# Kernel tuning notes

Measured on AMD Instinct MI355X. Metric: run time of the kernel, lower is better.

The kernel has to match this reference:

```python
import jax, jax.numpy as jnp
import numpy as np

IN_DIM = 256
HIDDEN = 512
MEM = 256
IN_LEN = 4096
THETA = 4096.0
BATCH = 32


def _expm(M):
    # scaling-and-squaring with Taylor series (float64)
    nrm = max(np.linalg.norm(M, 1), 1e-30)
    s = max(0, int(np.ceil(np.log2(nrm))) + 1)
    A = M / (2.0 ** s)
    d = M.shape[0]
    E = np.eye(d)
    term = np.eye(d)
    for k in range(1, 30):
        term = term @ A / k
        E = E + term
    for _ in range(s):
        E = E @ E
    return E


def _gen_AB(memory_size, theta):
    Q = np.arange(memory_size, dtype=np.float64).reshape(-1, 1)
    R = (2 * Q + 1) / theta
    i, j = np.meshgrid(Q, Q, indexing='ij')
    A = np.where(i < j, -1.0, (-1.0) ** (i - j + 1)) * R
    B = (-1.0) ** Q * R  # [mem, 1]
    # ZOH discretization with dt=1: expm of augmented [[A,B],[0,0]]
    d = memory_size
    em = np.zeros((d + 1, d + 1))
    em[:d, :d] = A
    em[:d, d:] = B
    ed = _expm(em)
    Ad = ed[:d, :d]
    Bd = ed[:d, d:]
    return Ad, Bd


def _impulse(memory_size, in_len, theta):
    Ad, Bd = _gen_AB(memory_size, theta)
    H = np.empty((memory_size, in_len), dtype=np.float64)
    v = Bd.copy()  # [mem, 1]
    for t in range(in_len):
        H[:, t] = v[:, 0]
        v = Ad @ v
    return H.astype(np.float32)


def setup_inputs() -> dict:
    key = jax.random.key(0)
    kx, ku, kh = jax.random.split(key, 3)
    x = jax.random.normal(kx, (BATCH, IN_LEN, IN_DIM), dtype=jnp.float32)
    W_u = jax.random.normal(ku, (1, IN_DIM), dtype=jnp.float32)
    W_h = jax.random.normal(kh, (HIDDEN, MEM + IN_DIM), dtype=jnp.float32)
    H = jnp.asarray(_impulse(MEM, IN_LEN, THETA))  # [mem, in_len]
    return {"x": x, "W_u": W_u, "W_h": W_h, "H": H}


def reference(x, W_u, W_h, H):
    batch, n, _ = x.shape
    # encode: u = relu(x @ W_u^T)  -> [B, n, 1]
    u = jax.nn.relu(jnp.einsum('bni,oi->bno', x, W_u))
    # FFT long convolution with impulse response H
    u_fft = jnp.fft.rfft(u.transpose(0, 2, 1), n=2 * n, axis=-1)  # [B,1,n+1]
    H_fft = jnp.fft.rfft(H, n=2 * n, axis=-1)                      # [mem,n+1]
    m = jnp.fft.irfft(u_fft * H_fft[None], n=2 * n, axis=-1)       # [B,mem,2n]
    m = m[:, :, :n].transpose(0, 2, 1)                             # [B,n,mem]
    # output head: h = relu([m, x] @ W_h^T)
    input_h = jnp.concatenate((m, x), axis=-1)                     # [B,n,mem+in_dim]
    h = jax.nn.relu(jnp.einsum('bnc,oc->bno', input_h, W_h))       # [B,n,hidden]
    h_n = h[:, -1, :]
    return (h, h_n)
```

## Files before the change

### kernel.cpp

```cpp
#include <hip/hip_runtime.h>
#include <hip/hip_bf16.h>
#include <math.h>


#define BATCH 32
#define T     4096
#define IND   256
#define HID   512
#define MEM   256
#define FFT_N 8192
#define FFT_LOG 13
#define BT    131072

typedef __attribute__((ext_vector_type(8))) short short8;
typedef __attribute__((ext_vector_type(8))) _Float16 half8;
typedef __attribute__((ext_vector_type(4))) float f32x4;

__device__ inline short f2bf(float f) {
    unsigned u = __float_as_uint(f);
    unsigned r = (u + 0x7FFFu + ((u >> 16) & 1u)) >> 16;
    return (short)r;
}
__device__ inline short f2h(float f) {
    union { _Float16 h; short s; } u;
    u.h = (_Float16)f;
    return u.s;
}

__global__ __launch_bounds__(256) void relu_u_kernel(const float* __restrict__ x,
                                                     const float* __restrict__ Wu,
                                                     float* __restrict__ u) {
    int wave = threadIdx.x >> 6, lane = threadIdx.x & 63;
    int r = blockIdx.x * 4 + wave;
    const float4 xv = *(const float4*)(x + (size_t)r * IND + lane * 4);
    const float4 wv = *(const float4*)(Wu + lane * 4);
    float acc = xv.x * wv.x + xv.y * wv.y + xv.z * wv.z + xv.w * wv.w;
    for (int off = 32; off; off >>= 1) acc += __shfl_down(acc, off);
    if (lane == 0) u[r] = fmaxf(acc, 0.f);
}

__device__ void fft_fwd_r4(float* re, float* im) {
    __syncthreads();
    {
        const float fm = -(float)M_PI / 4096.f;
#pragma unroll
        for (int s = 0; s < 8; ++s) {
            int k = threadIdx.x + s * 512;
            float sn, cs; __sincosf(fm * (float)k, &sn, &cs);
            float ar = re[k], ai = im[k], br = re[k + 4096], bi = im[k + 4096];
            re[k] = ar + br; im[k] = ai + bi;
            float dr = ar - br, di = ai - bi;
            re[k + 4096] = cs * dr - sn * di;
            im[k + 4096] = cs * di + sn * dr;
        }
        __syncthreads();
    }
#pragma unroll
    for (int st = 10; st >= 0; st -= 2) {
        int q = 1 << st;
        float fm = -(float)M_PI / (float)(2 * q);
#pragma unroll
        for (int s = 0; s < 4; ++s) {
            int k = threadIdx.x + s * 512;
            int j = k & (q - 1);
            int i0 = ((k >> st) << (st + 2)) + j;
            float ar = re[i0],         ai = im[i0];
            float br = re[i0 + q],     bi = im[i0 + q];
            float cr = re[i0 + 2 * q], ci = im[i0 + 2 * q];
            float dr = re[i0 + 3 * q], di = im[i0 + 3 * q];
            float t0r = ar + cr, t0i = ai + ci;
            float t1r = ar - cr, t1i = ai - ci;
            float t2r = br + dr, t2i = bi + di;
            float t3r = bi - di, t3i = dr - br;
            float sn, cs; __sincosf(fm * (float)j, &sn, &cs);
            float w2r = cs * cs - sn * sn, w2i = 2.f * cs * sn;
            float w3r = w2r * cs - w2i * sn, w3i = w2r * sn + w2i * cs;
            re[i0] = t0r + t2r;               im[i0] = t0i + t2i;
            float er = t0r - t2r, ei = t0i - t2i;
            re[i0 + q] = er * w2r - ei * w2i; im[i0 + q] = er * w2i + ei * w2r;
            float fr = t1r + t3r, fi = t1i + t3i;
            re[i0 + 2 * q] = fr * cs - fi * sn; im[i0 + 2 * q] = fr * sn + fi * cs;
            float gr = t1r - t3r, gi = t1i - t3i;
            re[i0 + 3 * q] = gr * w3r - gi * w3i; im[i0 + 3 * q] = gr * w3i + gi * w3r;
        }
        __syncthreads();
    }
}
__device__ void fft_inv_r4(float* re, float* im) {
    __syncthreads();
#pragma unroll
    for (int st = 0; st <= 10; st += 2) {
        int q = 1 << st;
        float fm = (float)M_PI / (float)(2 * q);
#pragma unroll
        for (int s = 0; s < 4; ++s) {
            int k = threadIdx.x + s * 512;
            int j = k & (q - 1);
            int i0 = ((k >> st) << (st + 2)) + j;
            float Ar = re[i0],         Ai = im[i0];
            float Br = re[i0 + q],     Bi = im[i0 + q];
            float Cr = re[i0 + 2 * q], Ci = im[i0 + 2 * q];
            float Dr = re[i0 + 3 * q], Di = im[i0 + 3 * q];
            float sn, cs; __sincosf(fm * (float)j, &sn, &cs);
            float w2r = cs * cs - sn * sn, w2i = 2.f * cs * sn;
            float w3r = w2r * cs - w2i * sn, w3i = w2r * sn + w2i * cs;
            float bpr = Br * w2r - Bi * w2i, bpi = Br * w2i + Bi * w2r;
            float cpr = Cr * cs - Ci * sn,   cpi = Cr * sn + Ci * cs;
            float dpr = Dr * w3r - Di * w3i, dpi = Dr * w3i + Di * w3r;
            float t0r = Ar + bpr, t0i = Ai + bpi;
            float t2r = Ar - bpr, t2i = Ai - bpi;
            float t1r = cpr + dpr, t1i = cpi + dpi;
            float t3r = cpr - dpr, t3i = cpi - dpi;
            re[i0]         = t0r + t1r; im[i0]         = t0i + t1i;
            re[i0 + 2 * q] = t0r - t1r; im[i0 + 2 * q] = t0i - t1i;
            re[i0 + q]     = t2r - t3i; im[i0 + q]     = t2i + t3r;
            re[i0 + 3 * q] = t2r + t3i; im[i0 + 3 * q] = t2i - t3r;
        }
        __syncthreads();
    }
    {
        const float fm = (float)M_PI / 4096.f;
#pragma unroll
        for (int s = 0; s < 8; ++s) {
            int k = threadIdx.x + s * 512;
            float sn, cs; __sincosf(fm * (float)k, &sn, &cs);
            float br = re[k + 4096], bi = im[k + 4096];
            float tr = cs * br - sn * bi, ti = cs * bi + sn * br;
            float ar = re[k], ai = im[k];
            re[k] = ar + tr;        im[k] = ai + ti;
            re[k + 4096] = ar - tr; im[k + 4096] = ai - ti;
        }
        __syncthreads();
    }
}

__global__ __launch_bounds__(512) void fwd_all_kernel(const float* __restrict__ u,
                                                      const float* __restrict__ H,
                                                      float2* __restrict__ Uf,
                                                      float2* __restrict__ Hf) {
    __shared__ float re[FFT_N];
    __shared__ float im[FFT_N];
    int r = blockIdx.x;
    const float* src = (r < BATCH) ? (u + (size_t)r * T) : (H + (size_t)(r - BATCH) * T);
    float2* dst = (r < BATCH) ? (Uf + (size_t)r * FFT_N) : (Hf + (size_t)(r - BATCH) * FFT_N);
    for (int i = threadIdx.x; i < FFT_N; i += 512) {
        re[i] = (i < T) ? src[i] : 0.f;
        im[i] = 0.f;
    }
    fft_fwd_r4(re, im);
    for (int i = threadIdx.x; i < FFT_N; i += 512) dst[i] = make_float2(re[i], im[i]);
}

__global__ __launch_bounds__(512) void conv_m_kernel(const float2* __restrict__ Uf,
                                                     const float2* __restrict__ Hf,
                                                     float* __restrict__ mT) {
    int p = blockIdx.x;
    int b = blockIdx.y;
    __shared__ float re[FFT_N];
    __shared__ float im[FFT_N];
    const float2* Ub = Uf + (size_t)b * FFT_N;
    const float2* H0 = Hf + (size_t)(2 * p) * FFT_N;
    const float2* H1 = Hf + (size_t)(2 * p + 1) * FFT_N;
    for (int f = threadIdx.x; f < FFT_N; f += 512) {
        float2 uv = Ub[f], h0 = H0[f], h1 = H1[f];
        float gr = h0.x - h1.y, gi = h0.y + h1.x;
        re[f] = uv.x * gr - uv.y * gi;
        im[f] = uv.x * gi + uv.y * gr;
    }
    fft_inv_r4(re, im);
    const float inv = 1.0f / (float)FFT_N;
    float* m0 = mT + (size_t)(2 * p) * BT + (size_t)b * T;
    float* m1 = mT + (size_t)(2 * p + 1) * BT + (size_t)b * T;
    for (int t = threadIdx.x; t < T; t += 512) {
        m0[t] = re[t] * inv;
        m1[t] = im[t] * inv;
    }
}

__global__ __launch_bounds__(256) void h_gemm_kernel(const float* __restrict__ x,
                                                     const float* __restrict__ Wh,
                                                     const float* __restrict__ mT,
                                                     float* __restrict__ out) {
    __shared__ __align__(16) short Asl[4][128][8];
    __shared__ __align__(16) short Bsl[4][128][8];
    int bn = blockIdx.x;
    int bm = blockIdx.y;
    int t = threadIdx.x;
    int wv = t >> 6, lane = t & 63;
    int wm = (wv & 1) * 64, wn = (wv >> 1) * 64;
    int ln = lane & 15, kg = lane >> 4;

    f32x4 acc[4][4] = {};
    int mrow = t >> 1, khalf = t & 1;
    for (int kc = 0; kc < HID; kc += 32) {
        float va[16];
        if (kc < MEM) {
            const float* mb = mT + (size_t)(kc + khalf * 16) * BT + (size_t)bm * 128 + mrow;
#pragma unroll
            for (int d = 0; d < 16; ++d) va[d] = mb[(size_t)d * BT];
        } else {
            const float* xr = x + (size_t)(bm * 128 + mrow) * IND + (kc - MEM) + khalf * 16;
            float4 v0 = *(const float4*)(xr + 0);
            float4 v1 = *(const float4*)(xr + 4);
            float4 v2 = *(const float4*)(xr + 8);
            float4 v3 = *(const float4*)(xr + 12);
            va[0] = v0.x; va[1] = v0.y; va[2] = v0.z; va[3] = v0.w;
            va[4] = v1.x; va[5] = v1.y; va[6] = v1.z; va[7] = v1.w;
            va[8] = v2.x; va[9] = v2.y; va[10] = v2.z; va[11] = v2.w;
            va[12] = v3.x; va[13] = v3.y; va[14] = v3.z; va[15] = v3.w;
        }
        short8 s0 = { f2h(va[0]), f2h(va[1]), f2h(va[2]), f2h(va[3]),
                      f2h(va[4]), f2h(va[5]), f2h(va[6]), f2h(va[7]) };
        short8 s1 = { f2h(va[8]), f2h(va[9]), f2h(va[10]), f2h(va[11]),
                      f2h(va[12]), f2h(va[13]), f2h(va[14]), f2h(va[15]) };
        const float* wr = Wh + (size_t)(bn * 128 + mrow) * HID + kc + khalf * 16;
        float4 w0 = *(const float4*)(wr + 0);
        float4 w1 = *(const float4*)(wr + 4);
        float4 w2 = *(const float4*)(wr + 8);
        float4 w3 = *(const float4*)(wr + 12);
        short8 b0 = { f2h(w0.x), f2h(w0.y), f2h(w0.z), f2h(w0.w),
                      f2h(w1.x), f2h(w1.y), f2h(w1.z), f2h(w1.w) };
        short8 b1 = { f2h(w2.x), f2h(w2.y), f2h(w2.z), f2h(w2.w),
                      f2h(w3.x), f2h(w3.y), f2h(w3.z), f2h(w3.w) };
        __syncthreads();
        *(short8*)&Asl[khalf * 2 + 0][mrow][0] = s0;
        *(short8*)&Asl[khalf * 2 + 1][mrow][0] = s1;
        *(short8*)&Bsl[khalf * 2 + 0][mrow][0] = b0;
        *(short8*)&Bsl[khalf * 2 + 1][mrow][0] = b1;
        __syncthreads();
        half8 af[4], bfr[4];
#pragma unroll
        for (int i = 0; i < 4; ++i) af[i] = *(half8*)&Asl[kg][wm + i * 16 + ln][0];
#pragma unroll
        for (int j = 0; j < 4; ++j) bfr[j] = *(half8*)&Bsl[kg][wn + j * 16 + ln][0];
#pragma unroll
        for (int i = 0; i < 4; ++i)
#pragma unroll
            for (int j = 0; j < 4; ++j)
                acc[i][j] = __builtin_amdgcn_mfma_f32_16x16x32_f16(af[i], bfr[j], acc[i][j], 0, 0, 0);
    }
#pragma unroll
    for (int i = 0; i < 4; ++i) {
#pragma unroll
        for (int j = 0; j < 4; ++j) {
#pragma unroll
            for (int r = 0; r < 4; ++r) {
                int row = bm * 128 + wm + i * 16 + (lane >> 4) * 4 + r;
                int col = bn * 128 + wn + j * 16 + ln;
                float v = fmaxf(acc[i][j][r], 0.f);
                out[(size_t)row * HID + col] = v;
                if ((row & (T - 1)) == (T - 1))
                    out[(size_t)BATCH * T * HID + (size_t)(row >> 12) * HID + col] = v;
            }
        }
    }
}

__device__ void fft_dif_fwd(float* re, float* im) {
    __syncthreads();
    for (int st = FFT_LOG; st >= 1; --st) {
        int half = 1 << (st - 1);
        float fm = -(float)M_PI / (float)half;
        for (int k = threadIdx.x; k < FFT_N / 2; k += 512) {
            int j  = k & (half - 1);
            int i1 = ((k >> (st - 1)) << st) + j;
            int i2 = i1 + half;
            float sn, cs;
            __sincosf(fm * (float)j, &sn, &cs);
            float ar = re[i1], ai = im[i1];
            float br = re[i2], bi = im[i2];
            re[i1] = ar + br; im[i1] = ai + bi;
            float dr = ar - br, di = ai - bi;
            re[i2] = cs * dr - sn * di;
            im[i2] = cs * di + sn * dr;
        }
        __syncthreads();
    }
}
__device__ void fft_dit_inv(float* re, float* im) {
    __syncthreads();
    for (int st = 1; st <= FFT_LOG; ++st) {
        int half = 1 << (st - 1);
        float fm = (float)M_PI / (float)half;
        for (int k = threadIdx.x; k < FFT_N / 2; k += 512) {
            int j  = k & (half - 1);
            int i1 = ((k >> (st - 1)) << st) + j;
            int i2 = i1 + half;
            float sn, cs;
            __sincosf(fm * (float)j, &sn, &cs);
            float br = re[i2], bi = im[i2];
            float tr = cs * br - sn * bi;
            float ti = cs * bi + sn * br;
            float ar = re[i1], ai = im[i1];
            re[i1] = ar + tr; im[i1] = ai + ti;
            re[i2] = ar - tr; im[i2] = ai - ti;
        }
        __syncthreads();
    }
}
__global__ __launch_bounds__(512) void fft_u_kernel(const float* __restrict__ u,
                                                    float2* __restrict__ Uf) {
    int b = blockIdx.x;
    __shared__ float re[FFT_N];
    __shared__ float im[FFT_N];
    for (int i = threadIdx.x; i < FFT_N; i += 512) {
        re[i] = i < T ? u[(size_t)b * T + i] : 0.f;
        im[i] = 0.f;
    }
    fft_dif_fwd(re, im);
    for (int i = threadIdx.x; i < FFT_N; i += 512)
        Uf[(size_t)b * FFT_N + i] = make_float2(re[i], im[i]);
}
__global__ __launch_bounds__(512) void g_fft_kernel(const float* __restrict__ Wh,
                                                    const float* __restrict__ H,
                                                    float2* __restrict__ Gf) {
    int o = blockIdx.x;
    __shared__ float re[FFT_N];
    __shared__ float im[FFT_N];
    const float* wrow = Wh + (size_t)o * HID;
    float acc[8];
#pragma unroll
    for (int d = 0; d < 8; ++d) acc[d] = 0.f;
    for (int q = 0; q < 256; ++q) {
        float w = wrow[q];
        const float* hrow = H + (size_t)q * T;
#pragma unroll
        for (int d = 0; d < 8; ++d)
            acc[d] = fmaf(w, hrow[threadIdx.x + d * 512], acc[d]);
    }
#pragma unroll
    for (int d = 0; d < 8; ++d) {
        re[threadIdx.x + d * 512] = acc[d];
        im[threadIdx.x + d * 512] = 0.f;
    }
    for (int i = T + threadIdx.x; i < FFT_N; i += 512) { re[i] = 0.f; im[i] = 0.f; }
    fft_dif_fwd(re, im);
    for (int i = threadIdx.x; i < FFT_N; i += 512)
        Gf[(size_t)o * FFT_N + i] = make_float2(re[i], im[i]);
}
__global__ __launch_bounds__(256) void xw_gemm_kernel(const float* __restrict__ x,
                                                      const float* __restrict__ Wh,
                                                      float* __restrict__ out) {
    __shared__ __align__(16) short Asl[4][128][8];
    __shared__ __align__(16) short Bsl[4][128][8];
    int bn = blockIdx.x;
    int bm = blockIdx.y;
    int t = threadIdx.x;
    int wv = t >> 6, lane = t & 63;
    int wm = (wv & 1) * 64, wn = (wv >> 1) * 64;
    int ln = lane & 15, kg = lane >> 4;
    f32x4 acc[4][4] = {};
    int mrow = t >> 1, khalf = t & 1;
    for (int kc = 0; kc < IND; kc += 32) {
        {
            const float* xr = x + ((size_t)(bm * 128 + mrow)) * IND + kc + khalf * 16;
            float4 v0 = *(const float4*)(xr + 0);
            float4 v1 = *(const float4*)(xr + 4);
            float4 v2 = *(const float4*)(xr + 8);
            float4 v3 = *(const float4*)(xr + 12);
            short8 s0 = { f2bf(v0.x), f2bf(v0.y), f2bf(v0.z), f2bf(v0.w),
                          f2bf(v1.x), f2bf(v1.y), f2bf(v1.z), f2bf(v1.w) };
            short8 s1 = { f2bf(v2.x), f2bf(v2.y), f2bf(v2.z), f2bf(v2.w),
                          f2bf(v3.x), f2bf(v3.y), f2bf(v3.z), f2bf(v3.w) };
            const float* wr = Wh + ((size_t)(bn * 128 + mrow)) * HID + 256 + kc + khalf * 16;
            float4 w0 = *(const float4*)(wr + 0);
            float4 w1 = *(const float4*)(wr + 4);
            float4 w2 = *(const float4*)(wr + 8);
            float4 w3 = *(const float4*)(wr + 12);
            short8 b0 = { f2bf(w0.x), f2bf(w0.y), f2bf(w0.z), f2bf(w0.w),
                          f2bf(w1.x), f2bf(w1.y), f2bf(w1.z), f2bf(w1.w) };
            short8 b1 = { f2bf(w2.x), f2bf(w2.y), f2bf(w2.z), f2bf(w2.w),
                          f2bf(w3.x), f2bf(w3.y), f2bf(w3.z), f2bf(w3.w) };
            __syncthreads();
            *(short8*)&Asl[khalf * 2 + 0][mrow][0] = s0;
            *(short8*)&Asl[khalf * 2 + 1][mrow][0] = s1;
            *(short8*)&Bsl[khalf * 2 + 0][mrow][0] = b0;
            *(short8*)&Bsl[khalf * 2 + 1][mrow][0] = b1;
            __syncthreads();
        }
        short8 af[4], bf[4];
#pragma unroll
        for (int i = 0; i < 4; ++i) af[i] = *(short8*)&Asl[kg][wm + i * 16 + ln][0];
#pragma unroll
        for (int j = 0; j < 4; ++j) bf[j] = *(short8*)&Bsl[kg][wn + j * 16 + ln][0];
#pragma unroll
        for (int i = 0; i < 4; ++i)
#pragma unroll
            for (int j = 0; j < 4; ++j)
                acc[i][j] = __builtin_amdgcn_mfma_f32_16x16x32_bf16(af[i], bf[j], acc[i][j], 0, 0, 0);
    }
#pragma unroll
    for (int i = 0; i < 4; ++i) {
#pragma unroll
        for (int j = 0; j < 4; ++j) {
#pragma unroll
            for (int r = 0; r < 4; ++r) {
                int row = bm * 128 + wm + i * 16 + (lane >> 4) * 4 + r;
                int col = bn * 128 + wn + j * 16 + (lane & 15);
                out[(size_t)row * HID + col] = acc[i][j][r];
            }
        }
    }
}
__global__ __launch_bounds__(512) void conv_apply_kernel(const float2* __restrict__ Uf,
                                                         const float2* __restrict__ Gf,
                                                         float* __restrict__ out) {
    int p = blockIdx.x;
    int b = blockIdx.y;
    __shared__ float re[FFT_N];
    __shared__ float im[FFT_N];
    const float2* Ub = Uf + (size_t)b * FFT_N;
    const float2* G0 = Gf + (size_t)(2 * p) * FFT_N;
    const float2* G1 = Gf + (size_t)(2 * p + 1) * FFT_N;
    for (int f = threadIdx.x; f < FFT_N; f += 512) {
        float2 uv = Ub[f], g0 = G0[f], g1 = G1[f];
        float gr = g0.x - g1.y, gi = g0.y + g1.x;
        re[f] = uv.x * gr - uv.y * gi;
        im[f] = uv.x * gi + uv.y * gr;
    }
    fft_dit_inv(re, im);
    const float inv = 1.0f / (float)FFT_N;
    for (int t = threadIdx.x; t < T; t += 512) {
        size_t idx = ((size_t)(b * T + t)) * HID + 2 * p;
        float2 xw = *(const float2*)(out + idx);
        float v0 = fmaxf(fmaf(re[t], inv, xw.x), 0.f);
        float v1 = fmaxf(fmaf(im[t], inv, xw.y), 0.f);
        *(float2*)(out + idx) = make_float2(v0, v1);
        if (t == T - 1) {
            size_t hn = (size_t)BATCH * T * HID + (size_t)b * HID + 2 * p;
            *(float2*)(out + hn) = make_float2(v0, v1);
        }
    }
}

extern "C" void kernel_launch(void* const* d_in, const int* in_sizes, int n_in,
                              void* d_out, int out_size, void* d_ws, size_t ws_size,
                              hipStream_t stream) {
    const float* x  = (const float*)d_in[0];
    const float* Wu = (const float*)d_in[1];
    const float* Wh = (const float*)d_in[2];
    const float* H  = (const float*)d_in[3];
    float* out = (float*)d_out;

    char* ws = (char*)d_ws;
    float* ws_u = (float*)ws;

    const size_t off_U  = 524288;
    const size_t off_Hf = off_U + 2097152;
    const size_t off_mT = off_Hf + 16777216;
    const size_t need   = off_mT + (size_t)MEM * BT * 4;

    relu_u_kernel<<<BATCH * T / 4, 256, 0, stream>>>(x, Wu, ws_u);

    if (ws_size >= need) {
        float2* ws_U  = (float2*)(ws + off_U);
        float2* ws_Hf = (float2*)(ws + off_Hf);
        float*  ws_mT = (float*)(ws + off_mT);
        fwd_all_kernel<<<BATCH + MEM, 512, 0, stream>>>(ws_u, H, ws_U, ws_Hf);
        conv_m_kernel<<<dim3(MEM / 2, BATCH), 512, 0, stream>>>(ws_U, ws_Hf, ws_mT);
        h_gemm_kernel<<<dim3(HID / 128, BT / 128), 256, 0, stream>>>(x, Wh, ws_mT, out);
    } else {
        float2* ws_U = (float2*)(ws + 524288);
        float2* ws_G = (float2*)(ws + 524288 + 2097152);
        fft_u_kernel<<<BATCH, 512, 0, stream>>>(ws_u, ws_U);
        g_fft_kernel<<<HID, 512, 0, stream>>>(Wh, H, ws_G);
        xw_gemm_kernel<<<dim3(HID / 128, BATCH * T / 128), 256, 0, stream>>>(x, Wh, out);
        conv_apply_kernel<<<dim3(HID / 2, BATCH), 512, 0, stream>>>(ws_U, ws_G, out);
    }
}
```

Measured before the change: 689.0 us.

## Store conv output and GEMM operands as packed fp16 and load MFMA fragments directly

```diff
diff --git a/kernel.cpp b/kernel.cpp
--- a/kernel.cpp
+++ b/kernel.cpp
@@ -21,22 +21,37 @@
     unsigned r = (u + 0x7FFFu + ((u >> 16) & 1u)) >> 16;
     return (short)r;
 }
-__device__ inline short f2h(float f) {
-    union { _Float16 h; short s; } u;
-    u.h = (_Float16)f;
-    return u.s;
+__device__ inline unsigned pk2h(float a, float b) {
+    union { _Float16 h[2]; unsigned u; } v;
+    v.h[0] = (_Float16)a; v.h[1] = (_Float16)b;
+    return v.u;
 }
 
 __global__ __launch_bounds__(256) void relu_u_kernel(const float* __restrict__ x,
                                                      const float* __restrict__ Wu,
-                                                     float* __restrict__ u) {
+                                                     float* __restrict__ u,
+                                                     _Float16* __restrict__ xh) {
     int wave = threadIdx.x >> 6, lane = threadIdx.x & 63;
     int r = blockIdx.x * 4 + wave;
     const float4 xv = *(const float4*)(x + (size_t)r * IND + lane * 4);
     const float4 wv = *(const float4*)(Wu + lane * 4);
+    union { _Float16 h[4]; uint2 u2; } hv;
+    hv.h[0] = (_Float16)xv.x; hv.h[1] = (_Float16)xv.y;
+    hv.h[2] = (_Float16)xv.z; hv.h[3] = (_Float16)xv.w;
+    *(uint2*)(xh + (size_t)r * IND + lane * 4) = hv.u2;
     float acc = xv.x * wv.x + xv.y * wv.y + xv.z * wv.z + xv.w * wv.w;
     for (int off = 32; off; off >>= 1) acc += __shfl_down(acc, off);
     if (lane == 0) u[r] = fmaxf(acc, 0.f);
+}
+
+__global__ __launch_bounds__(256) void wh_half_kernel(const float* __restrict__ Wh,
+                                                      _Float16* __restrict__ whf) {
+    int i = blockIdx.x * 256 + threadIdx.x;
+    float4 v = *(const float4*)(Wh + (size_t)i * 4);
+    union { _Float16 h[4]; uint2 u2; } hv;
+    hv.h[0] = (_Float16)v.x; hv.h[1] = (_Float16)v.y;
+    hv.h[2] = (_Float16)v.z; hv.h[3] = (_Float16)v.w;
+    *(uint2*)(whf + (size_t)i * 4) = hv.u2;
 }
 
 __device__ void fft_fwd_r4(float* re, float* im) {
@@ -55,7 +70,6 @@
         }
         __syncthreads();
     }
-#pragma unroll
     for (int st = 10; st >= 0; st -= 2) {
         int q = 1 << st;
         float fm = -(float)M_PI / (float)(2 * q);
@@ -88,7 +102,6 @@
 }
 __device__ void fft_inv_r4(float* re, float* im) {
     __syncthreads();
-#pragma unroll
     for (int st = 0; st <= 10; st += 2) {
         int q = 1 << st;
         float fm = (float)M_PI / (float)(2 * q);
@@ -153,91 +166,83 @@
 
 __global__ __launch_bounds__(512) void conv_m_kernel(const float2* __restrict__ Uf,
                                                      const float2* __restrict__ Hf,
-                                                     float* __restrict__ mT) {
-    int p = blockIdx.x;
-    int b = blockIdx.y;
+                                                     _Float16* __restrict__ m2) {
+    int qb = blockIdx.x;
+    int b  = blockIdx.y;
     __shared__ float re[FFT_N];
     __shared__ float im[FFT_N];
     const float2* Ub = Uf + (size_t)b * FFT_N;
-    const float2* H0 = Hf + (size_t)(2 * p) * FFT_N;
-    const float2* H1 = Hf + (size_t)(2 * p + 1) * FFT_N;
-    for (int f = threadIdx.x; f < FFT_N; f += 512) {
-        float2 uv = Ub[f], h0 = H0[f], h1 = H1[f];
-        float gr = h0.x - h1.y, gi = h0.y + h1.x;
-        re[f] = uv.x * gr - uv.y * gi;
-        im[f] = uv.x * gi + uv.y * gr;
-    }
-    fft_inv_r4(re, im);
     const float inv = 1.0f / (float)FFT_N;
-    float* m0 = mT + (size_t)(2 * p) * BT + (size_t)b * T;
-    float* m1 = mT + (size_t)(2 * p + 1) * BT + (size_t)b * T;
-    for (int t = threadIdx.x; t < T; t += 512) {
-        m0[t] = re[t] * inv;
-        m1[t] = im[t] * inv;
-    }
-}
-
-__global__ __launch_bounds__(256) void h_gemm_kernel(const float* __restrict__ x,
-                                                     const float* __restrict__ Wh,
-                                                     const float* __restrict__ mT,
+    unsigned p0[8], p1[8], p2[8], p3[8];
+
+#define DO_FF(FF, PK)                                                          \
+    {                                                                          \
+        const float2* Ha = Hf + (size_t)(qb * 8 + 2 * (FF)) * FFT_N;           \
+        const float2* Hb = Ha + FFT_N;                                         \
+        for (int f = threadIdx.x; f < FFT_N; f += 512) {                       \
+            float2 uv = Ub[f], h0 = Ha[f], h1 = Hb[f];                         \
+            float gr = h0.x - h1.y, gi = h0.y + h1.x;           \
+            re[f] = uv.x * gr - uv.y * gi;                                     \
+            im[f] = uv.x * gi + uv.y * gr;                                     \
+        }                                                                      \
+        fft_inv_r4(re, im);                                                    \
+        _Pragma("unroll")                                                      \
+        for (int it = 0; it < 8; ++it) {                                       \
+            int tt = threadIdx.x + it * 512;                                   \
+            PK[it] = pk2h(re[tt] * inv, im[tt] * inv);                         \
+        }                                                                      \
+    }
+
+    DO_FF(0, p0)
+    DO_FF(1, p1)
+    DO_FF(2, p2)
+    DO_FF(3, p3)
+#undef DO_FF
+
+    _Float16* dst = m2 + ((size_t)qb * BT + (size_t)b * T) * 8;
+#pragma unroll
+    for (int it = 0; it < 8; ++it) {
+        int tt = threadIdx.x + it * 512;
+        uint4 w;
+        w.x = p0[it]; w.y = p1[it]; w.z = p2[it]; w.w = p3[it];
+        *(uint4*)(dst + (size_t)tt * 8) = w;
+    }
+}
+
+__global__ __launch_bounds__(256) void h_gemm_kernel(const _Float16* __restrict__ xh,
+                                                     const _Float16* __restrict__ whf,
+                                                     const _Float16* __restrict__ m2,
                                                      float* __restrict__ out) {
-    __shared__ __align__(16) short Asl[4][128][8];
-    __shared__ __align__(16) short Bsl[4][128][8];
     int bn = blockIdx.x;
     int bm = blockIdx.y;
     int t = threadIdx.x;
     int wv = t >> 6, lane = t & 63;
     int wm = (wv & 1) * 64, wn = (wv >> 1) * 64;
     int ln = lane & 15, kg = lane >> 4;
+    int row0 = bm * 128 + wm + ln;
+    int col0 = bn * 128 + wn + ln;
 
     f32x4 acc[4][4] = {};
-    int mrow = t >> 1, khalf = t & 1;
+#pragma unroll
     for (int kc = 0; kc < HID; kc += 32) {
-        float va[16];
+        half8 af[4], bf[4];
         if (kc < MEM) {
-            const float* mb = mT + (size_t)(kc + khalf * 16) * BT + (size_t)bm * 128 + mrow;
-#pragma unroll
-            for (int d = 0; d < 16; ++d) va[d] = mb[(size_t)d * BT];
+#pragma unroll
+            for (int i = 0; i < 4; ++i)
+                af[i] = *(const half8*)(m2 + ((size_t)(kc / 8 + kg) * BT + row0 + i * 16) * 8);
         } else {
-            const float* xr = x + (size_t)(bm * 128 + mrow) * IND + (kc - MEM) + khalf * 16;
-            float4 v0 = *(const float4*)(xr + 0);
-            float4 v1 = *(const float4*)(xr + 4);
-            float4 v2 = *(const float4*)(xr + 8);
-            float4 v3 = *(const float4*)(xr + 12);
-            va[0] = v0.x; va[1] = v0.y; va[2] = v0.z; va[3] = v0.w;
-            va[4] = v1.x; va[5] = v1.y; va[6] = v1.z; va[7] = v1.w;
-            va[8] = v2.x; va[9] = v2.y; va[10] = v2.z; va[11] = v2.w;
-            va[12] = v3.x; va[13] = v3.y; va[14] = v3.z; va[15] = v3.w;
-        }
-        short8 s0 = { f2h(va[0]), f2h(va[1]), f2h(va[2]), f2h(va[3]),
-                      f2h(va[4]), f2h(va[5]), f2h(va[6]), f2h(va[7]) };
-        short8 s1 = { f2h(va[8]), f2h(va[9]), f2h(va[10]), f2h(va[11]),
-                      f2h(va[12]), f2h(va[13]), f2h(va[14]), f2h(va[15]) };
-        const float* wr = Wh + (size_t)(bn * 128 + mrow) * HID + kc + khalf * 16;
-        float4 w0 = *(const float4*)(wr + 0);
-        float4 w1 = *(const float4*)(wr + 4);
-        float4 w2 = *(const float4*)(wr + 8);
-        float4 w3 = *(const float4*)(wr + 12);
-        short8 b0 = { f2h(w0.x), f2h(w0.y), f2h(w0.z), f2h(w0.w),
-                      f2h(w1.x), f2h(w1.y), f2h(w1.z), f2h(w1.w) };
-        short8 b1 = { f2h(w2.x), f2h(w2.y), f2h(w2.z), f2h(w2.w),
-                      f2h(w3.x), f2h(w3.y), f2h(w3.z), f2h(w3.w) };
-        __syncthreads();
-        *(short8*)&Asl[khalf * 2 + 0][mrow][0] = s0;
-        *(short8*)&Asl[khalf * 2 + 1][mrow][0] = s1;
-        *(short8*)&Bsl[khalf * 2 + 0][mrow][0] = b0;
-        *(short8*)&Bsl[khalf * 2 + 1][mrow][0] = b1;
-        __syncthreads();
-        half8 af[4], bfr[4];
-#pragma unroll
-        for (int i = 0; i < 4; ++i) af[i] = *(half8*)&Asl[kg][wm + i * 16 + ln][0];
-#pragma unroll
-        for (int j = 0; j < 4; ++j) bfr[j] = *(half8*)&Bsl[kg][wn + j * 16 + ln][0];
+#pragma unroll
+            for (int i = 0; i < 4; ++i)
+                af[i] = *(const half8*)(xh + (size_t)(row0 + i * 16) * IND + (kc - MEM) + kg * 8);
+        }
+#pragma unroll
+        for (int j = 0; j < 4; ++j)
+            bf[j] = *(const half8*)(whf + (size_t)(col0 + j * 16) * HID + kc + kg * 8);
 #pragma unroll
         for (int i = 0; i < 4; ++i)
 #pragma unroll
             for (int j = 0; j < 4; ++j)
-                acc[i][j] = __builtin_amdgcn_mfma_f32_16x16x32_f16(af[i], bfr[j], acc[i][j], 0, 0, 0);
+                acc[i][j] = __builtin_amdgcn_mfma_f32_16x16x32_f16(af[i], bf[j], acc[i][j], 0, 0, 0);
     }
 #pragma unroll
     for (int i = 0; i < 4; ++i) {
@@ -245,7 +250,7 @@
         for (int j = 0; j < 4; ++j) {
 #pragma unroll
             for (int r = 0; r < 4; ++r) {
-                int row = bm * 128 + wm + i * 16 + (lane >> 4) * 4 + r;
+                int row = bm * 128 + wm + i * 16 + kg * 4 + r;
                 int col = bn * 128 + wn + j * 16 + ln;
                 float v = fmaxf(acc[i][j][r], 0.f);
                 out[(size_t)row * HID + col] = v;
@@ -443,25 +448,33 @@
     float* out = (float*)d_out;
 
     char* ws = (char*)d_ws;
-    float* ws_u = (float*)ws;
-
-    const size_t off_U  = 524288;
-    const size_t off_Hf = off_U + 2097152;
-    const size_t off_mT = off_Hf + 16777216;
-    const size_t need   = off_mT + (size_t)MEM * BT * 4;
-
-    relu_u_kernel<<<BATCH * T / 4, 256, 0, stream>>>(x, Wu, ws_u);
+
+    const size_t off_u   = 0;
+    const size_t off_xh  = off_u  + 524288;
+    const size_t off_whf = off_xh + 67108864;
+    const size_t off_U   = off_whf + 524288;
+    const size_t off_Hf  = off_U  + 2097152;
+    const size_t off_m2  = off_Hf + 16777216;
+    const size_t need    = off_m2 + (size_t)MEM * BT * 2;
 
     if (ws_size >= need) {
-        float2* ws_U  = (float2*)(ws + off_U);
-        float2* ws_Hf = (float2*)(ws + off_Hf);
-        float*  ws_mT = (float*)(ws + off_mT);
+        float*     ws_u   = (float*)(ws + off_u);
+        _Float16*  ws_xh  = (_Float16*)(ws + off_xh);
+        _Float16*  ws_whf = (_Float16*)(ws + off_whf);
+        float2*    ws_U   = (float2*)(ws + off_U);
+        float2*    ws_Hf  = (float2*)(ws + off_Hf);
+        _Float16*  ws_m2  = (_Float16*)(ws + off_m2);
+
+        wh_half_kernel<<<HID * HID / 4 / 256, 256, 0, stream>>>(Wh, ws_whf);
+        relu_u_kernel<<<BT / 4, 256, 0, stream>>>(x, Wu, ws_u, ws_xh);
         fwd_all_kernel<<<BATCH + MEM, 512, 0, stream>>>(ws_u, H, ws_U, ws_Hf);
-        conv_m_kernel<<<dim3(MEM / 2, BATCH), 512, 0, stream>>>(ws_U, ws_Hf, ws_mT);
-        h_gemm_kernel<<<dim3(HID / 128, BT / 128), 256, 0, stream>>>(x, Wh, ws_mT, out);
+        conv_m_kernel<<<dim3(MEM / 8, BATCH), 512, 0, stream>>>(ws_U, ws_Hf, ws_m2);
+        h_gemm_kernel<<<dim3(HID / 128, BT / 128), 256, 0, stream>>>(ws_xh, ws_whf, ws_m2, out);
     } else {
+        float*  ws_u = (float*)ws;
         float2* ws_U = (float2*)(ws + 524288);
         float2* ws_G = (float2*)(ws + 524288 + 2097152);
+        relu_u_kernel<<<BT / 4, 256, 0, stream>>>(x, Wu, ws_u, (_Float16*)(ws + 524288 + 2097152 + 33554432));
         fft_u_kernel<<<BATCH, 512, 0, stream>>>(ws_u, ws_U);
         g_fft_kernel<<<HID, 512, 0, stream>>>(Wh, H, ws_G);
         xw_gemm_kernel<<<dim3(HID / 128, BATCH * T / 128), 256, 0, stream>>>(x, Wh, out);
```

After: 740.6 us. 1.07x slower.
